# Kernel optimization log

Hardware: AMD Instinct MI355X
Metric: run time of the kernel (lower is better)

Reference implementation:

```python
import jax, jax.numpy as jnp
import numpy as np

B, S, D, O = 8, 2048, 1024, 1024  # batch, seq_len, state_dim(=input_dim), output_dim


def setup_inputs() -> dict:
    key = jax.random.key(0)
    k_in, k_a, k_bc = jax.random.split(key, 3)
    inputs = jax.random.normal(k_in, (B, S, D), dtype=jnp.float32)
    # Stable diagonal transition (|A| < 1) so the 2048-step recurrence stays bounded.
    A = jax.random.uniform(k_a, (D,), minval=-0.99, maxval=0.99, dtype=jnp.float32)
    BC = jax.random.normal(k_bc, (D, O), dtype=jnp.float32) / D
    return {"inputs": inputs, "A": A, "BC": BC}


def reference(inputs, A, BC):
    # Diagonal LTI recurrence: h_t = A * h_{t-1} + x_t ; out_t = h_t @ BC
    # h0 = zeros (the module's h0 Parameter is initialized to zeros).
    x_tfirst = jnp.swapaxes(inputs, 0, 1)  # [S, B, D]

    def step(h, x_t):
        h = h * A + x_t
        return h, h

    h0 = jnp.zeros((inputs.shape[0], A.shape[0]), dtype=inputs.dtype)
    _, hs = jax.lax.scan(step, h0, x_tfirst)  # hs: [S, B, D]
    # Single fused projection over all timesteps instead of per-step matmuls.
    out = jnp.einsum('sbd,do->bso', hs, BC)  # [B, S, O]
    return out
```

## Files before the change

kernel.cpp:

```cpp
#include <hip/hip_runtime.h>
#include <hip/hip_bf16.h>

#define BB 8
#define SS 2048
#define DD 1024
#define OO 1024
#define MM (BB * SS)
#define KK DD
#define NN OO
#define CC 64
#define LL 32

typedef __bf16 bf16x8 __attribute__((ext_vector_type(8)));
typedef __bf16 bf16x4 __attribute__((ext_vector_type(4)));
typedef float floatx4 __attribute__((ext_vector_type(4)));

__device__ __forceinline__ float4 fma4(float4 h, float4 a, float4 v) {
    h.x = fmaf(h.x, a.x, v.x);
    h.y = fmaf(h.y, a.y, v.y);
    h.z = fmaf(h.z, a.z, v.z);
    h.w = fmaf(h.w, a.w, v.w);
    return h;
}

__global__ __launch_bounds__(256) void prep(const float* __restrict__ x,
                                            const float* __restrict__ A,
                                            float* __restrict__ carry,
                                            const float* __restrict__ BC,
                                            __bf16* __restrict__ BCt) {
    __shared__ float tile[32][33];
    const int id = blockIdx.x;
    if (id < BB * CC) {
        const int c = id & (CC - 1);
        const int b = id >> 6;
        const int i4 = threadIdx.x;
        const float4 a = ((const float4*)A)[i4];
        const float4* xp = (const float4*)(x + ((size_t)b * SS + (size_t)c * LL) * DD) + i4;
        float4 h = make_float4(0.f, 0.f, 0.f, 0.f);
#pragma unroll
        for (int t0 = 0; t0 < LL; t0 += 8) {
            float4 v[8];
#pragma unroll
            for (int u = 0; u < 8; ++u) v[u] = xp[(size_t)(t0 + u) * (DD / 4)];
#pragma unroll
            for (int u = 0; u < 8; ++u) h = fma4(h, a, v[u]);
        }
        ((float4*)carry)[((size_t)b * CC + c) * (DD / 4) + i4] = h;
    } else {
        const int t = id - BB * CC;
        const int o0 = (t & 31) * 32;
        const int d0 = (t >> 5) * 32;
        const int tx = threadIdx.x & 31;
        const int ty = threadIdx.x >> 5;
#pragma unroll
        for (int i = 0; i < 4; ++i) {
            const int dd = ty + i * 8;
            tile[dd][tx] = BC[(size_t)(d0 + dd) * OO + o0 + tx];
        }
        __syncthreads();
#pragma unroll
        for (int i = 0; i < 4; ++i) {
            const int oo = ty + i * 8;
            BCt[(size_t)(o0 + oo) * DD + d0 + tx] = (__bf16)tile[tx][oo];
        }
    }
}

__global__ __launch_bounds__(256) void chunk_scan(const float* __restrict__ carry,
                                                  const float* __restrict__ A,
                                                  float* __restrict__ Hprev) {
    const int idx = blockIdx.x * 256 + threadIdx.x;
    const int d = idx & (DD - 1);
    const int b = idx >> 10;
    const float a = A[d];
    float aL = a;
#pragma unroll
    for (int i = 0; i < 5; ++i) aL *= aL;
    float ca[CC];
#pragma unroll
    for (int c = 0; c < CC; ++c)
        ca[c] = carry[((size_t)b * CC + c) * DD + d];
    float h = 0.f;
#pragma unroll
    for (int c = 0; c < CC; ++c) {
        Hprev[((size_t)b * CC + c) * DD + d] = h;
        h = fmaf(aL, h, ca[c]);
    }
}

__global__ __launch_bounds__(256) void scan_emit(const float* __restrict__ x,
                                                 const float* __restrict__ A,
                                                 const float* __restrict__ Hprev,
                                                 __bf16* __restrict__ hs) {
    const int id = blockIdx.x;
    const int c = id & (CC - 1);
    const int b = id >> 6;
    const int i4 = threadIdx.x;
    const float4 a = ((const float4*)A)[i4];
    float4 h = ((const float4*)Hprev)[((size_t)b * CC + c) * (DD / 4) + i4];
    const size_t base = ((size_t)b * SS + (size_t)c * LL) * DD;
    const float4* xp = (const float4*)(x + base) + i4;
    bf16x4* hp = (bf16x4*)(hs + base) + i4;
#pragma unroll
    for (int t0 = 0; t0 < LL; t0 += 8) {
        float4 v[8];
#pragma unroll
        for (int u = 0; u < 8; ++u) v[u] = xp[(size_t)(t0 + u) * (DD / 4)];
#pragma unroll
        for (int u = 0; u < 8; ++u) {
            h = fma4(h, a, v[u]);
            bf16x4 o;
            o[0] = (__bf16)h.x; o[1] = (__bf16)h.y; o[2] = (__bf16)h.z; o[3] = (__bf16)h.w;
            hp[(size_t)(t0 + u) * (DD / 4)] = o;
        }
    }
}

#define TM 128
#define TN 128
#define TK 32

__device__ __forceinline__ void async16(void* lds, const void* g) {
    __builtin_amdgcn_global_load_lds(
        (__attribute__((address_space(1))) void*)(void*)g,
        (__attribute__((address_space(3))) void*)lds, 16, 0, 0);
}

__global__ __launch_bounds__(256) void gemm_bt(const __bf16* __restrict__ Am,
                                               const __bf16* __restrict__ Bt,
                                               float* __restrict__ C) {
    __shared__ __align__(16) __bf16 As[TM * TK];
    __shared__ __align__(16) __bf16 Bs[TN * TK];

    const int tid = threadIdx.x;
    const int wave = tid >> 6;
    const int lane = tid & 63;
    const int wm = (wave >> 1) * 64;
    const int wn = (wave & 1) * 64;
    const int lanelo = lane & 15;
    const int quad = lane >> 4;
    const int tile_m = blockIdx.x * TM;
    const int tile_n = blockIdx.y * TN;

    const int cid0 = tid;
    const int cid1 = tid + 256;
    const int r0 = cid0 >> 2, q0 = (cid0 & 3) * 8;
    const int r1 = cid1 >> 2, q1 = (cid1 & 3) * 8;

    floatx4 acc[4][4];
#pragma unroll
    for (int i = 0; i < 4; ++i)
#pragma unroll
        for (int j = 0; j < 4; ++j) acc[i][j] = (floatx4){0.f, 0.f, 0.f, 0.f};

    for (int k0 = 0; k0 < KK; k0 += TK) {
        __syncthreads();
        async16(&As[cid0 * 8], Am + (size_t)(tile_m + r0) * KK + k0 + q0);
        async16(&As[cid1 * 8], Am + (size_t)(tile_m + r1) * KK + k0 + q1);
        async16(&Bs[cid0 * 8], Bt + (size_t)(tile_n + r0) * KK + k0 + q0);
        async16(&Bs[cid1 * 8], Bt + (size_t)(tile_n + r1) * KK + k0 + q1);
        __syncthreads();

        bf16x8 af[4], bf[4];
#pragma unroll
        for (int i = 0; i < 4; ++i)
            af[i] = *(const bf16x8*)(&As[(wm + i * 16 + lanelo) * TK + quad * 8]);
#pragma unroll
        for (int j = 0; j < 4; ++j)
            bf[j] = *(const bf16x8*)(&Bs[(wn + j * 16 + lanelo) * TK + quad * 8]);

#pragma unroll
        for (int i = 0; i < 4; ++i)
#pragma unroll
            for (int j = 0; j < 4; ++j)
                acc[i][j] = __builtin_amdgcn_mfma_f32_16x16x32_bf16(af[i], bf[j], acc[i][j], 0, 0, 0);
    }

#pragma unroll
    for (int i = 0; i < 4; ++i) {
        const int row = tile_m + wm + i * 16 + quad * 4;
#pragma unroll
        for (int r = 0; r < 4; ++r) {
            float* crow = C + (size_t)(row + r) * NN + tile_n + wn + lanelo;
#pragma unroll
            for (int j = 0; j < 4; ++j) crow[j * 16] = acc[i][j][r];
        }
    }
}

extern "C" void kernel_launch(void* const* d_in, const int* in_sizes, int n_in,
                              void* d_out, int out_size, void* d_ws, size_t ws_size,
                              hipStream_t stream) {
    const float* x  = (const float*)d_in[0];
    const float* A  = (const float*)d_in[1];
    const float* BC = (const float*)d_in[2];
    float* out = (float*)d_out;

    char* ws = (char*)d_ws;
    __bf16* hs   = (__bf16*)ws;
    float* carry = (float*)(ws + 33554432);
    float* Hprev = (float*)(ws + 33554432 + 2097152);
    __bf16* BCt  = (__bf16*)(ws + 33554432 + 4194304);

    prep<<<dim3(BB * CC + 1024), 256, 0, stream>>>(x, A, carry, BC, BCt);
    chunk_scan<<<dim3(BB * DD / 256), 256, 0, stream>>>(carry, A, Hprev);
    scan_emit<<<dim3(BB * CC), 256, 0, stream>>>(x, A, Hprev, hs);
    gemm_bt<<<dim3(MM / TM, NN / TN), 256, 0, stream>>>(hs, BCt, out);
}
```

Baseline: 179.0 us.

## Fold chunk-carry scan into emit kernel and double-buffer GEMM LDS tiles

Removes the separate chunk_scan kernel. Each scan_emit block now recomputes its starting state by serially combining the carries of all earlier chunks, using A to the power of the chunk length. This saves a launch and the Hprev buffer, but adds redundant carry reads and a serial dependency chain of up to 63 steps per block. Separately, the bf16 GEMM now double-buffers its LDS tiles and issues async loads for the next K-step before computing the current one, so global loads overlap MFMA work and one barrier per iteration is dropped.

```diff
diff --git a/kernel.cpp b/kernel.cpp
--- a/kernel.cpp
+++ b/kernel.cpp
@@ -66,38 +66,27 @@
     }
 }
 
-__global__ __launch_bounds__(256) void chunk_scan(const float* __restrict__ carry,
-                                                  const float* __restrict__ A,
-                                                  float* __restrict__ Hprev) {
-    const int idx = blockIdx.x * 256 + threadIdx.x;
-    const int d = idx & (DD - 1);
-    const int b = idx >> 10;
-    const float a = A[d];
-    float aL = a;
-#pragma unroll
-    for (int i = 0; i < 5; ++i) aL *= aL;
-    float ca[CC];
-#pragma unroll
-    for (int c = 0; c < CC; ++c)
-        ca[c] = carry[((size_t)b * CC + c) * DD + d];
-    float h = 0.f;
-#pragma unroll
-    for (int c = 0; c < CC; ++c) {
-        Hprev[((size_t)b * CC + c) * DD + d] = h;
-        h = fmaf(aL, h, ca[c]);
-    }
-}
-
 __global__ __launch_bounds__(256) void scan_emit(const float* __restrict__ x,
                                                  const float* __restrict__ A,
-                                                 const float* __restrict__ Hprev,
+                                                 const float* __restrict__ carry,
                                                  __bf16* __restrict__ hs) {
     const int id = blockIdx.x;
     const int c = id & (CC - 1);
     const int b = id >> 6;
     const int i4 = threadIdx.x;
     const float4 a = ((const float4*)A)[i4];
-    float4 h = ((const float4*)Hprev)[((size_t)b * CC + c) * (DD / 4) + i4];
+    float4 aL = a;
+#pragma unroll
+    for (int i = 0; i < 5; ++i) { aL.x *= aL.x; aL.y *= aL.y; aL.z *= aL.z; aL.w *= aL.w; }
+    float4 h = make_float4(0.f, 0.f, 0.f, 0.f);
+    const float4* cp = (const float4*)carry + (size_t)b * CC * (DD / 4) + i4;
+    for (int j = 0; j < c; ++j) {
+        const float4 cv = cp[(size_t)j * (DD / 4)];
+        h.x = fmaf(h.x, aL.x, cv.x);
+        h.y = fmaf(h.y, aL.y, cv.y);
+        h.z = fmaf(h.z, aL.z, cv.z);
+        h.w = fmaf(h.w, aL.w, cv.w);
+    }
     const size_t base = ((size_t)b * SS + (size_t)c * LL) * DD;
     const float4* xp = (const float4*)(x + base) + i4;
     bf16x4* hp = (bf16x4*)(hs + base) + i4;
@@ -119,6 +108,7 @@
 #define TM 128
 #define TN 128
 #define TK 32
+#define NITER (KK / TK)
 
 __device__ __forceinline__ void async16(void* lds, const void* g) {
     __builtin_amdgcn_global_load_lds(
@@ -129,8 +119,8 @@
 __global__ __launch_bounds__(256) void gemm_bt(const __bf16* __restrict__ Am,
                                                const __bf16* __restrict__ Bt,
                                                float* __restrict__ C) {
-    __shared__ __align__(16) __bf16 As[TM * TK];
-    __shared__ __align__(16) __bf16 Bs[TN * TK];
+    __shared__ __align__(16) __bf16 As[2][TM * TK];
+    __shared__ __align__(16) __bf16 Bs[2][TN * TK];
 
     const int tid = threadIdx.x;
     const int wave = tid >> 6;
@@ -147,33 +137,47 @@
     const int r0 = cid0 >> 2, q0 = (cid0 & 3) * 8;
     const int r1 = cid1 >> 2, q1 = (cid1 & 3) * 8;
 
+    const __bf16* Ab = Am + (size_t)(tile_m + r0) * KK + q0;
+    const __bf16* Ab1 = Am + (size_t)(tile_m + r1) * KK + q1;
+    const __bf16* Bb = Bt + (size_t)(tile_n + r0) * KK + q0;
+    const __bf16* Bb1 = Bt + (size_t)(tile_n + r1) * KK + q1;
+
     floatx4 acc[4][4];
 #pragma unroll
     for (int i = 0; i < 4; ++i)
 #pragma unroll
         for (int j = 0; j < 4; ++j) acc[i][j] = (floatx4){0.f, 0.f, 0.f, 0.f};
 
-    for (int k0 = 0; k0 < KK; k0 += TK) {
+    async16(&As[0][cid0 * 8], Ab);
+    async16(&As[0][cid1 * 8], Ab1);
+    async16(&Bs[0][cid0 * 8], Bb);
+    async16(&Bs[0][cid1 * 8], Bb1);
+
+    int cur = 0;
+    for (int i = 0; i < NITER; ++i) {
         __syncthreads();
-        async16(&As[cid0 * 8], Am + (size_t)(tile_m + r0) * KK + k0 + q0);
-        async16(&As[cid1 * 8], Am + (size_t)(tile_m + r1) * KK + k0 + q1);
-        async16(&Bs[cid0 * 8], Bt + (size_t)(tile_n + r0) * KK + k0 + q0);
-        async16(&Bs[cid1 * 8], Bt + (size_t)(tile_n + r1) * KK + k0 + q1);
-        __syncthreads();
+        if (i + 1 < NITER) {
+            const int k = (i + 1) * TK;
+            async16(&As[cur ^ 1][cid0 * 8], Ab + k);
+            async16(&As[cur ^ 1][cid1 * 8], Ab1 + k);
+            async16(&Bs[cur ^ 1][cid0 * 8], Bb + k);
+            async16(&Bs[cur ^ 1][cid1 * 8], Bb1 + k);
+        }
 
         bf16x8 af[4], bf[4];
 #pragma unroll
-        for (int i = 0; i < 4; ++i)
-            af[i] = *(const bf16x8*)(&As[(wm + i * 16 + lanelo) * TK + quad * 8]);
+        for (int ii = 0; ii < 4; ++ii)
+            af[ii] = *(const bf16x8*)(&As[cur][(wm + ii * 16 + lanelo) * TK + quad * 8]);
 #pragma unroll
         for (int j = 0; j < 4; ++j)
-            bf[j] = *(const bf16x8*)(&Bs[(wn + j * 16 + lanelo) * TK + quad * 8]);
-
-#pragma unroll
-        for (int i = 0; i < 4; ++i)
+            bf[j] = *(const bf16x8*)(&Bs[cur][(wn + j * 16 + lanelo) * TK + quad * 8]);
+
+#pragma unroll
+        for (int ii = 0; ii < 4; ++ii)
 #pragma unroll
             for (int j = 0; j < 4; ++j)
-                acc[i][j] = __builtin_amdgcn_mfma_f32_16x16x32_bf16(af[i], bf[j], acc[i][j], 0, 0, 0);
+                acc[ii][j] = __builtin_amdgcn_mfma_f32_16x16x32_bf16(af[ii], bf[j], acc[ii][j], 0, 0, 0);
+        cur ^= 1;
     }
 
 #pragma unroll
@@ -199,11 +203,9 @@
     char* ws = (char*)d_ws;
     __bf16* hs   = (__bf16*)ws;
     float* carry = (float*)(ws + 33554432);
-    float* Hprev = (float*)(ws + 33554432 + 2097152);
-    __bf16* BCt  = (__bf16*)(ws + 33554432 + 4194304);
+    __bf16* BCt  = (__bf16*)(ws + 33554432 + 2097152);
 
     prep<<<dim3(BB * CC + 1024), 256, 0, stream>>>(x, A, carry, BC, BCt);
-    chunk_scan<<<dim3(BB * DD / 256), 256, 0, stream>>>(carry, A, Hprev);
-    scan_emit<<<dim3(BB * CC), 256, 0, stream>>>(x, A, Hprev, hs);
+    scan_emit<<<dim3(BB * CC), 256, 0, stream>>>(x, A, carry, hs);
     gemm_bt<<<dim3(MM / TM, NN / TN), 256, 0, stream>>>(hs, BCt, out);
 }
```

Result: no change. 179.0 us (-0.0%).
